# Kernel tuning notes

Measured on AMD Instinct MI355X. Metric: run time of the kernel, lower is better.

Reference implementation:

```python
import jax, jax.numpy as jnp
import numpy as np

N, DEG, D_IN, D_HID = 50000, 16, 963, 256


def setup_inputs() -> dict:
    key = jax.random.key(0)
    ks = jax.random.split(key, 8)
    s = 0.02
    neighbours = jax.random.randint(ks[0], (N, DEG), 0, N)
    shape_features = jax.random.normal(ks[1], (N, D_IN), dtype=jnp.float32)
    # layer 0: D_IN -> D_HID; layers 1..13 (stacked): D_HID -> D_HID; extra: D_HID -> 3
    W_self0 = jax.random.normal(ks[2], (D_IN, D_HID), dtype=jnp.float32) * s
    W_neigh0 = jax.random.normal(ks[3], (D_IN, D_HID), dtype=jnp.float32) * s
    b0 = jnp.zeros((D_HID,), jnp.float32)
    W_self = jax.random.normal(ks[4], (13, D_HID, D_HID), dtype=jnp.float32) * s
    W_neigh = jax.random.normal(ks[5], (13, D_HID, D_HID), dtype=jnp.float32) * s
    b = jnp.zeros((13, D_HID), jnp.float32)
    W_extra = jax.random.normal(ks[6], (D_HID, 3), dtype=jnp.float32) * s
    b_extra = jnp.zeros((3,), jnp.float32)
    return {
        "neighbours": neighbours,
        "shape_features": shape_features,
        "W_self0": W_self0, "W_neigh0": W_neigh0, "b0": b0,
        "W_self": W_self, "W_neigh": W_neigh, "b": b,
        "W_extra": W_extra, "b_extra": b_extra,
    }


def _gcn(x, neighbours, Ws, Wn, bias):
    # gather neighbour features [N, DEG, D] and sum-aggregate, plus self transform
    agg = jnp.take(x, neighbours, axis=0).sum(axis=1)
    return x @ Ws + agg @ Wn + bias


def reference(neighbours, shape_features, W_self0, W_neigh0, b0, W_self, W_neigh, b, W_extra, b_extra):
    x = jax.nn.relu(_gcn(shape_features, neighbours, W_self0, W_neigh0, b0))
    for i in range(6):  # 6 residual blocks of 2 GCN layers each
        temp = x
        x = jax.nn.relu(_gcn(x, neighbours, W_self[2 * i], W_neigh[2 * i], b[2 * i]))
        x = jax.nn.relu(_gcn(x, neighbours, W_self[2 * i + 1], W_neigh[2 * i + 1], b[2 * i + 1]))
        x = (temp + x) / 2
    x = jax.nn.relu(_gcn(x, neighbours, W_self[12], W_neigh[12], b[12]))
    coordinates = x @ W_extra + b_extra  # extra layer called without neighbours -> linear
    return (x, coordinates)
```

## Files before the change

### kernel.cpp

```cpp
#include <hip/hip_runtime.h>
#include <hip/hip_bf16.h>
#include <hip/hip_fp16.h>
#include <stdint.h>

#define NNODES 50000
#define NPAD   50048
#define DEG    16
#define DIN    963
#define K0PAD  992
#define DHID   256
#define SCALE  (1.0f / 1024.0f)
#define ISCALE 1024.0f

typedef __attribute__((ext_vector_type(4))) float    f32x4;
typedef __attribute__((ext_vector_type(8))) _Float16 f16x8;
typedef __attribute__((ext_vector_type(4))) _Float16 f16x4;

typedef const __attribute__((address_space(1))) void GV;
typedef __attribute__((address_space(3))) void LV;

__device__ __forceinline__ void gl2lds16(const void* g, void* l) {
    __builtin_amdgcn_global_load_lds((GV*)g, (LV*)l, 16, 0, 0);
}

__global__ __launch_bounds__(256) void gemm_dual0(
    const _Float16* __restrict__ A, int K,
    const _Float16* __restrict__ Wp,
    _Float16* __restrict__ ys, _Float16* __restrict__ yn)
{
    __shared__ _Float16 lds[2][2][4096];

    const int tid  = threadIdx.x;
    const int w    = tid >> 6;
    const int lane = tid & 63;
    const int bm   = blockIdx.x * 128;
    const int nb   = blockIdx.y * 128;

    const int KT = K >> 5;

    auto stage = [&](int s, int kt) {
        const int k0 = kt << 5;
#pragma unroll
        for (int i = 0; i < 2; ++i) {
            const int j   = w + (i << 2);
            const int c   = (j << 6) + lane;
            const int row = c & 127;
            const int k8  = (c >> 7) << 3;
            gl2lds16(A  + (size_t)(bm + row) * K + k0 + k8, &lds[s][0][(size_t)j << 9]);
            gl2lds16(Wp + (size_t)(nb + row) * K + k0 + k8, &lds[s][1][(size_t)j << 9]);
        }
    };

    const int wm = (w >> 1) << 6;
    const int wn = (w & 1) << 6;
    const int lr = lane & 15;
    const int kh = lane >> 4;

    f32x4 acc[4][4] = {};

    stage(0, 0);
    __syncthreads();
    int cur = 0;
    for (int kt = 0; kt < KT; ++kt) {
        if (kt + 1 < KT) stage(cur ^ 1, kt + 1);
        f16x8 a[4], b[4];
#pragma unroll
        for (int mi = 0; mi < 4; ++mi)
            a[mi] = *(const f16x8*)&lds[cur][0][((kh << 7) + wm + (mi << 4) + lr) << 3];
#pragma unroll
        for (int ni = 0; ni < 4; ++ni)
            b[ni] = *(const f16x8*)&lds[cur][1][((kh << 7) + wn + (ni << 4) + lr) << 3];
#pragma unroll
        for (int mi = 0; mi < 4; ++mi)
#pragma unroll
            for (int ni = 0; ni < 4; ++ni)
                acc[mi][ni] = __builtin_amdgcn_mfma_f32_16x16x32_f16(a[mi], b[ni], acc[mi][ni], 0, 0, 0);
        __syncthreads();
        cur ^= 1;
    }

    _Float16* C = (blockIdx.y < 2) ? ys : yn;
    const int cb = (nb & 255) + wn;
#pragma unroll
    for (int mi = 0; mi < 4; ++mi) {
        const size_t rbase = (size_t)(bm + wm + (mi << 4) + (kh << 2)) << 8;
#pragma unroll
        for (int ni = 0; ni < 4; ++ni) {
            const int col = cb + (ni << 4) + lr;
#pragma unroll
            for (int r = 0; r < 4; ++r)
                C[rbase + ((size_t)r << 8) + col] = (_Float16)acc[mi][ni][r];
        }
    }
}

template<int FINAL>
__global__ __launch_bounds__(256) void gemm_fused(
    const _Float16* __restrict__ X, const _Float16* __restrict__ AG,
    const _Float16* __restrict__ W, const float* __restrict__ bias,
    const _Float16* __restrict__ res,
    _Float16* __restrict__ outh, float* __restrict__ outf)
{
    __shared__ _Float16 ldsA[2][2048];
    __shared__ _Float16 ldsB[2][8192];

    const int tid  = threadIdx.x;
    const int w    = tid >> 6;
    const int lane = tid & 63;

    const int nwg = gridDim.x, bid = blockIdx.x;
    const int q = nwg >> 3, r_ = nwg & 7, xc = bid & 7;
    const int wgid = (xc < r_ ? xc * (q + 1) : r_ * (q + 1) + (xc - r_) * q) + (bid >> 3);
    const int bm = wgid << 6;

    auto stage = [&](int s, int kt) {
        const _Float16* src = (kt < 8) ? X : AG;
        const int kl = (kt & 7) << 5;
        {
            const int c = tid;
            gl2lds16(src + (size_t)(bm + (c & 63)) * 256 + kl + ((c >> 6) << 3),
                     &ldsA[s][(size_t)w << 9]);
        }
#pragma unroll
        for (int i = 0; i < 4; ++i) {
            const int j = (i << 2) + w;
            const int c = (j << 6) + lane;
            gl2lds16(W + (size_t)(c & 255) * 512 + (kt << 5) + ((c >> 8) << 3),
                     &ldsB[s][(size_t)j << 9]);
        }
    };

    const int wn = w << 6;
    const int lr = lane & 15;
    const int k4 = lane >> 4;

    f32x4 acc[4][4] = {};

    stage(0, 0);
    __syncthreads();
    int cur = 0;
    for (int kt = 0; kt < 16; ++kt) {
        if (kt + 1 < 16) stage(cur ^ 1, kt + 1);
        f16x8 a[4], b[4];
#pragma unroll
        for (int mi = 0; mi < 4; ++mi)
            a[mi] = *(const f16x8*)&ldsA[cur][((k4 << 6) + (mi << 4) + lr) << 3];
#pragma unroll
        for (int ni = 0; ni < 4; ++ni)
            b[ni] = *(const f16x8*)&ldsB[cur][((k4 << 8) + wn + (ni << 4) + lr) << 3];
#pragma unroll
        for (int mi = 0; mi < 4; ++mi)
#pragma unroll
            for (int ni = 0; ni < 4; ++ni)
                acc[mi][ni] = __builtin_amdgcn_mfma_f32_16x16x32_f16(a[mi], b[ni], acc[mi][ni], 0, 0, 0);
        __syncthreads();
        cur ^= 1;
    }

    const int r0 = k4 << 2;
#pragma unroll
    for (int mi = 0; mi < 4; ++mi) {
        const int grow0 = bm + (mi << 4) + r0;
#pragma unroll
        for (int ni = 0; ni < 4; ++ni) {
            const int col = wn + (ni << 4) + lr;
            const float bcol = bias[col] * SCALE;
#pragma unroll
            for (int r = 0; r < 4; ++r) {
                const int grow = grow0 + r;
                float s = acc[mi][ni][r] + bcol;
                s = fmaxf(s, 0.f);
                if (res) s = ((float)res[((size_t)grow << 8) + col] + s) * 0.5f;
                if (FINAL) {
                    if (grow < NNODES) outf[((size_t)grow << 8) + col] = s * ISCALE;
                } else {
                    outh[((size_t)grow << 8) + col] = (_Float16)s;
                }
            }
        }
    }
}

__global__ __launch_bounds__(256) void gather_sum(
    const _Float16* __restrict__ x, const int* __restrict__ nbr,
    _Float16* __restrict__ agg)
{
    const int w    = threadIdx.x >> 6;
    const int lane = threadIdx.x & 63;
    const int n    = (blockIdx.x << 2) + w;
    const int c4   = lane << 2;

    const int* nr = nbr + n * DEG;
    float s0 = 0.f, s1 = 0.f, s2 = 0.f, s3 = 0.f;
#pragma unroll
    for (int j = 0; j < DEG; ++j) {
        const f16x4 v = *(const f16x4*)(x + (((size_t)nr[j]) << 8) + c4);
        s0 += (float)v[0]; s1 += (float)v[1]; s2 += (float)v[2]; s3 += (float)v[3];
    }
    f16x4 o;
    o[0] = (_Float16)s0; o[1] = (_Float16)s1; o[2] = (_Float16)s2; o[3] = (_Float16)s3;
    *(f16x4*)(agg + (((size_t)n) << 8) + c4) = o;
}

__global__ __launch_bounds__(256) void combine0(
    const _Float16* __restrict__ ys, const _Float16* __restrict__ yn,
    const int* __restrict__ nbr, const float* __restrict__ bias,
    _Float16* __restrict__ outh)
{
    const int w    = threadIdx.x >> 6;
    const int lane = threadIdx.x & 63;
    const int n    = (blockIdx.x << 2) + w;
    const int c4   = lane << 2;
    const size_t base = ((size_t)n << 8) + c4;

    const f16x4 ysv = *(const f16x4*)(ys + base);
    const float4 bv = *(const float4*)(bias + c4);
    float s0 = (float)ysv[0] + bv.x * SCALE;
    float s1 = (float)ysv[1] + bv.y * SCALE;
    float s2 = (float)ysv[2] + bv.z * SCALE;
    float s3 = (float)ysv[3] + bv.w * SCALE;

    const int* nr = nbr + n * DEG;
#pragma unroll
    for (int j = 0; j < DEG; ++j) {
        const f16x4 v = *(const f16x4*)(yn + (((size_t)nr[j]) << 8) + c4);
        s0 += (float)v[0]; s1 += (float)v[1]; s2 += (float)v[2]; s3 += (float)v[3];
    }
    f16x4 o;
    o[0] = (_Float16)fmaxf(s0, 0.f); o[1] = (_Float16)fmaxf(s1, 0.f);
    o[2] = (_Float16)fmaxf(s2, 0.f); o[3] = (_Float16)fmaxf(s3, 0.f);
    *(f16x4*)(outh + base) = o;
}

__global__ __launch_bounds__(64) void coords_kernel(
    const float* __restrict__ x, const float* __restrict__ We,
    const float* __restrict__ be, float* __restrict__ out3, int N)
{
    const int n = blockIdx.x;
    const int l = threadIdx.x;
    const float4 xv = *(const float4*)(x + (size_t)n * 256 + l * 4);
    float p0 = 0.f, p1 = 0.f, p2 = 0.f;
    const float xs[4] = {xv.x, xv.y, xv.z, xv.w};
#pragma unroll
    for (int i = 0; i < 4; ++i) {
        const int cidx = l * 4 + i;
        p0 += xs[i] * We[cidx * 3 + 0];
        p1 += xs[i] * We[cidx * 3 + 1];
        p2 += xs[i] * We[cidx * 3 + 2];
    }
#pragma unroll
    for (int off = 32; off > 0; off >>= 1) {
        p0 += __shfl_down(p0, off);
        p1 += __shfl_down(p1, off);
        p2 += __shfl_down(p2, off);
    }
    if (l == 0) {
        out3[(size_t)n * 3 + 0] = p0 + be[0];
        out3[(size_t)n * 3 + 1] = p1 + be[1];
        out3[(size_t)n * 3 + 2] = p2 + be[2];
    }
}

__global__ __launch_bounds__(256) void conv_sf(const float* __restrict__ sf,
                                               _Float16* __restrict__ sfb)
{
    const int idx = blockIdx.x * 256 + threadIdx.x;
    const int row = idx / 124;
    const int k8  = (idx % 124) << 3;
    f16x8 o = {};
    if (row < NNODES) {
#pragma unroll
        for (int i = 0; i < 8; ++i) {
            const int k = k8 + i;
            o[i] = (k < DIN) ? (_Float16)(sf[(size_t)row * DIN + k] * SCALE) : (_Float16)0.f;
        }
    }
    *(f16x8*)(sfb + (size_t)row * K0PAD + k8) = o;
}

__global__ __launch_bounds__(256) void pack_w0(const float* __restrict__ Ws0,
                                               const float* __restrict__ Wn0,
                                               _Float16* __restrict__ Wp0)
{
    const int idx = blockIdx.x * 256 + threadIdx.x;
    const int nn  = idx & 511;
    const int k8  = idx >> 9;
    const float* W = (nn < 256) ? Ws0 : Wn0;
    const int n0 = nn & 255;
    f16x8 o;
#pragma unroll
    for (int i = 0; i < 8; ++i) {
        const int k = (k8 << 3) + i;
        o[i] = (k < DIN) ? (_Float16)W[(size_t)k * 256 + n0] : (_Float16)0.f;
    }
    *(f16x8*)(Wp0 + (size_t)nn * K0PAD + (k8 << 3)) = o;
}

__global__ __launch_bounds__(256) void pack_w2(const float* __restrict__ Ws,
                                               const float* __restrict__ Wn,
                                               _Float16* __restrict__ Wpk2)
{
    const int idx = blockIdx.x * 256 + threadIdx.x;
    const int n   = idx & 255;
    const int k8  = (idx >> 8) & 63;
    const int l   = idx >> 14;
    f16x8 o;
#pragma unroll
    for (int i = 0; i < 8; ++i) {
        const int k = (k8 << 3) + i;
        const float* W = (k < 256) ? Ws : Wn;
        o[i] = (_Float16)W[(size_t)l * 65536 + (k & 255) * 256 + n];
    }
    *(f16x8*)(Wpk2 + (size_t)l * 131072 + (size_t)n * 512 + (k8 << 3)) = o;
}

extern "C" void kernel_launch(void* const* d_in, const int* in_sizes, int n_in,
                              void* d_out, int out_size, void* d_ws, size_t ws_size,
                              hipStream_t stream)
{
    const int*   nbr = (const int*)d_in[0];
    const float* sf  = (const float*)d_in[1];
    const float* Ws0 = (const float*)d_in[2];
    const float* Wn0 = (const float*)d_in[3];
    const float* b0  = (const float*)d_in[4];
    const float* Ws  = (const float*)d_in[5];
    const float* Wn  = (const float*)d_in[6];
    const float* bb  = (const float*)d_in[7];
    const float* We  = (const float*)d_in[8];
    const float* be  = (const float*)d_in[9];
    float* out = (float*)d_out;

    uint8_t* w = (uint8_t*)d_ws;
    _Float16* sfb  = (_Float16*)w;
    _Float16* P    = (_Float16*)w;
    _Float16* Q    = P + (size_t)NPAD * 256;
    _Float16* Wpk2 = Q + (size_t)NPAD * 256;
    _Float16* Wp0  = (_Float16*)(w + (size_t)NPAD * K0PAD * 2);
    _Float16* ysb  = Wp0 + (size_t)512 * K0PAD;
    _Float16* ynb  = ysb + (size_t)NPAD * 256;
    _Float16* agg  = ysb;

    conv_sf<<<NPAD * 124 / 256, 256, 0, stream>>>(sf, sfb);
    pack_w0<<<512 * 124 / 256, 256, 0, stream>>>(Ws0, Wn0, Wp0);

    gemm_dual0<<<dim3(NPAD / 128, 4), 256, 0, stream>>>(sfb, K0PAD, Wp0, ysb, ynb);
    pack_w2<<<13 * 64 * 256 / 256, 256, 0, stream>>>(Ws, Wn, Wpk2);
    combine0<<<NNODES / 4, 256, 0, stream>>>(ysb, ynb, nbr, b0, P);

    const int fg = NPAD / 64;

    for (int t = 0; t < 6; ++t) {
        const int lA = 2 * t, lB = lA + 1;
        gather_sum<<<NNODES / 4, 256, 0, stream>>>(P, nbr, agg);
        gemm_fused<0><<<fg, 256, 0, stream>>>(P, agg, Wpk2 + (size_t)lA * 131072,
                                              bb + lA * 256, nullptr, Q, nullptr);
        gather_sum<<<NNODES / 4, 256, 0, stream>>>(Q, nbr, agg);
        gemm_fused<0><<<fg, 256, 0, stream>>>(Q, agg, Wpk2 + (size_t)lB * 131072,
                                              bb + lB * 256, P, P, nullptr);
    }

    gather_sum<<<NNODES / 4, 256, 0, stream>>>(P, nbr, agg);
    gemm_fused<1><<<fg, 256, 0, stream>>>(P, agg, Wpk2 + (size_t)12 * 131072,
                                          bb + 12 * 256, nullptr, nullptr, out);

    coords_kernel<<<NNODES, 64, 0, stream>>>(out, We, be, out + (size_t)NNODES * 256, NNODES);
}
```

Before: 1.826 ms.

## Fuse neighbour gather-sum into the GEMM A-tile staging and enlarge row tiles

```diff
diff --git a/kernel.cpp b/kernel.cpp
--- a/kernel.cpp
+++ b/kernel.cpp
@@ -95,44 +95,55 @@
 }
 
 template<int FINAL>
-__global__ __launch_bounds__(256) void gemm_fused(
-    const _Float16* __restrict__ X, const _Float16* __restrict__ AG,
+__global__ __launch_bounds__(512) void fused_layer(
+    const _Float16* __restrict__ X, const int* __restrict__ nbr,
     const _Float16* __restrict__ W, const float* __restrict__ bias,
     const _Float16* __restrict__ res,
     _Float16* __restrict__ outh, float* __restrict__ outf)
 {
-    __shared__ _Float16 ldsA[2][2048];
+    __shared__ _Float16 ldsA[2][4096];
     __shared__ _Float16 ldsB[2][8192];
 
     const int tid  = threadIdx.x;
     const int w    = tid >> 6;
     const int lane = tid & 63;
-
-    const int nwg = gridDim.x, bid = blockIdx.x;
-    const int q = nwg >> 3, r_ = nwg & 7, xc = bid & 7;
-    const int wgid = (xc < r_ ? xc * (q + 1) : r_ * (q + 1) + (xc - r_) * q) + (bid >> 3);
-    const int bm = wgid << 6;
+    const int bm   = blockIdx.x << 7;
+
+    const int growg = bm + (tid >> 2);
+    const int nrow  = (growg < NNODES) ? growg : (NNODES - 1);
+    const int4* np  = (const int4*)(nbr + nrow * DEG);
+    const int4 q0 = np[0], q1 = np[1], q2 = np[2], q3 = np[3];
+    const int kq = (tid & 3) << 3;
 
     auto stage = [&](int s, int kt) {
-        const _Float16* src = (kt < 8) ? X : AG;
-        const int kl = (kt & 7) << 5;
-        {
+        if (kt < 8) {
             const int c = tid;
-            gl2lds16(src + (size_t)(bm + (c & 63)) * 256 + kl + ((c >> 6) << 3),
-                     &ldsA[s][(size_t)w << 9]);
-        }
-#pragma unroll
-        for (int i = 0; i < 4; ++i) {
-            const int j = (i << 2) + w;
-            const int c = (j << 6) + lane;
-            gl2lds16(W + (size_t)(c & 255) * 512 + (kt << 5) + ((c >> 8) << 3),
-                     &ldsB[s][(size_t)j << 9]);
+            gl2lds16(X + ((size_t)(bm + (c & 127)) << 8) + (kt << 5) + ((c >> 7) << 3),
+                     &ldsA[s][(size_t)c << 3]);
+        } else {
+            const int kl = ((kt & 7) << 5) + kq;
+            auto LD = [&](int r) -> f16x8 {
+                return *(const f16x8*)(X + ((size_t)r << 8) + kl);
+            };
+            const f16x8 t0 = (LD(q0.x) + LD(q0.y)) + (LD(q0.z) + LD(q0.w));
+            const f16x8 t1 = (LD(q1.x) + LD(q1.y)) + (LD(q1.z) + LD(q1.w));
+            const f16x8 t2 = (LD(q2.x) + LD(q2.y)) + (LD(q2.z) + LD(q2.w));
+            const f16x8 t3 = (LD(q3.x) + LD(q3.y)) + (LD(q3.z) + LD(q3.w));
+            const f16x8 sum = (t0 + t1) + (t2 + t3);
+            *(f16x8*)&ldsA[s][(size_t)(((tid & 3) << 7) + (tid >> 2)) << 3] = sum;
+        }
+#pragma unroll
+        for (int i = 0; i < 2; ++i) {
+            const int c = (i << 9) + tid;
+            gl2lds16(W + ((size_t)(c & 255) << 9) + (kt << 5) + ((c >> 8) << 3),
+                     &ldsB[s][(size_t)c << 3]);
         }
     };
 
-    const int wn = w << 6;
+    const int wm = (w >> 2) << 6;
+    const int wn = (w & 3) << 6;
     const int lr = lane & 15;
-    const int k4 = lane >> 4;
+    const int kh = lane >> 4;
 
     f32x4 acc[4][4] = {};
 
@@ -144,10 +155,10 @@
         f16x8 a[4], b[4];
 #pragma unroll
         for (int mi = 0; mi < 4; ++mi)
-            a[mi] = *(const f16x8*)&ldsA[cur][((k4 << 6) + (mi << 4) + lr) << 3];
+            a[mi] = *(const f16x8*)&ldsA[cur][((kh << 7) + wm + (mi << 4) + lr) << 3];
 #pragma unroll
         for (int ni = 0; ni < 4; ++ni)
-            b[ni] = *(const f16x8*)&ldsB[cur][((k4 << 8) + wn + (ni << 4) + lr) << 3];
+            b[ni] = *(const f16x8*)&ldsB[cur][((kh << 8) + wn + (ni << 4) + lr) << 3];
 #pragma unroll
         for (int mi = 0; mi < 4; ++mi)
 #pragma unroll
@@ -157,10 +168,10 @@
         cur ^= 1;
     }
 
-    const int r0 = k4 << 2;
+    const int r0 = kh << 2;
 #pragma unroll
     for (int mi = 0; mi < 4; ++mi) {
-        const int grow0 = bm + (mi << 4) + r0;
+        const int grow0 = bm + wm + (mi << 4) + r0;
 #pragma unroll
         for (int ni = 0; ni < 4; ++ni) {
             const int col = wn + (ni << 4) + lr;
@@ -181,27 +192,6 @@
     }
 }
 
-__global__ __launch_bounds__(256) void gather_sum(
-    const _Float16* __restrict__ x, const int* __restrict__ nbr,
-    _Float16* __restrict__ agg)
-{
-    const int w    = threadIdx.x >> 6;
-    const int lane = threadIdx.x & 63;
-    const int n    = (blockIdx.x << 2) + w;
-    const int c4   = lane << 2;
-
-    const int* nr = nbr + n * DEG;
-    float s0 = 0.f, s1 = 0.f, s2 = 0.f, s3 = 0.f;
-#pragma unroll
-    for (int j = 0; j < DEG; ++j) {
-        const f16x4 v = *(const f16x4*)(x + (((size_t)nr[j]) << 8) + c4);
-        s0 += (float)v[0]; s1 += (float)v[1]; s2 += (float)v[2]; s3 += (float)v[3];
-    }
-    f16x4 o;
-    o[0] = (_Float16)s0; o[1] = (_Float16)s1; o[2] = (_Float16)s2; o[3] = (_Float16)s3;
-    *(f16x4*)(agg + (((size_t)n) << 8) + c4) = o;
-}
-
 __global__ __launch_bounds__(256) void combine0(
     const _Float16* __restrict__ ys, const _Float16* __restrict__ yn,
     const int* __restrict__ nbr, const float* __restrict__ bias,
@@ -338,7 +328,6 @@
     _Float16* Wp0  = (_Float16*)(w + (size_t)NPAD * K0PAD * 2);
     _Float16* ysb  = Wp0 + (size_t)512 * K0PAD;
     _Float16* ynb  = ysb + (size_t)NPAD * 256;
-    _Float16* agg  = ysb;
 
     conv_sf<<<NPAD * 124 / 256, 256, 0, stream>>>(sf, sfb);
     pack_w0<<<512 * 124 / 256, 256, 0, stream>>>(Ws0, Wn0, Wp0);
@@ -347,21 +336,18 @@
     pack_w2<<<13 * 64 * 256 / 256, 256, 0, stream>>>(Ws, Wn, Wpk2);
     combine0<<<NNODES / 4, 256, 0, stream>>>(ysb, ynb, nbr, b0, P);
 
-    const int fg = NPAD / 64;
+    const int fg = NPAD / 128;
 
     for (int t = 0; t < 6; ++t) {
         const int lA = 2 * t, lB = lA + 1;
-        gather_sum<<<NNODES / 4, 256, 0, stream>>>(P, nbr, agg);
-        gemm_fused<0><<<fg, 256, 0, stream>>>(P, agg, Wpk2 + (size_t)lA * 131072,
-                                              bb + lA * 256, nullptr, Q, nullptr);
-        gather_sum<<<NNODES / 4, 256, 0, stream>>>(Q, nbr, agg);
-        gemm_fused<0><<<fg, 256, 0, stream>>>(Q, agg, Wpk2 + (size_t)lB * 131072,
-                                              bb + lB * 256, P, P, nullptr);
-    }
-
-    gather_sum<<<NNODES / 4, 256, 0, stream>>>(P, nbr, agg);
-    gemm_fused<1><<<fg, 256, 0, stream>>>(P, agg, Wpk2 + (size_t)12 * 131072,
-                                          bb + 12 * 256, nullptr, nullptr, out);
+        fused_layer<0><<<fg, 512, 0, stream>>>(P, nbr, Wpk2 + (size_t)lA * 131072,
+                                               bb + lA * 256, nullptr, Q, nullptr);
+        fused_layer<0><<<fg, 512, 0, stream>>>(Q, nbr, Wpk2 + (size_t)lB * 131072,
+                                               bb + lB * 256, P, P, nullptr);
+    }
+
+    fused_layer<1><<<fg, 512, 0, stream>>>(P, nbr, Wpk2 + (size_t)12 * 131072,
+                                           bb + 12 * 256, nullptr, nullptr, out);
 
     coords_kernel<<<NNODES, 64, 0, stream>>>(out, We, be, out + (size_t)NNODES * 256, NNODES);
 }
```

New measurement: 1.591 ms. 12.9% less time.
